# Performance work log

Hardware: AMD Instinct MI355X
Metric: run time of the kernel (lower is better)

The kernel has to match this reference:

```python
import jax, jax.numpy as jnp
import numpy as np

N_HEAD = 16
NEG_INF = -1e30  # finite mask value, safe for softmax/grad


def setup_inputs() -> dict:
    key = jax.random.key(0)
    k1, k2, k3 = jax.random.split(key, 3)
    B, T, C = 4, 2049, 1024
    x = jax.random.normal(k1, (B, T, C), dtype=jnp.float32)
    W_attn = jax.random.normal(k2, (C, 3 * C), dtype=jnp.float32) * (1.0 / np.sqrt(C))
    W_proj = jax.random.normal(k3, (C, C), dtype=jnp.float32) * (1.0 / np.sqrt(C))
    return {"x": x, "W_attn": W_attn, "W_proj": W_proj}


def reference(x, W_attn, W_proj):
    B, T, C = x.shape
    H = N_HEAD
    D = C // H
    qkv = x @ W_attn                                  # (B, T, 3C)
    q, k, v = jnp.split(qkv, 3, axis=-1)
    q = q.reshape(B, T, H, D).transpose(0, 2, 1, 3)   # (B, H, T, D)
    k = k.reshape(B, T, H, D).transpose(0, 2, 1, 3)
    v = v.reshape(B, T, H, D).transpose(0, 2, 1, 3)
    # hybrid mask: causal tril, but state token (row 0) attends to ALL positions
    mask = jnp.tril(jnp.ones((T, T), dtype=bool))
    mask = mask.at[0, :].set(True)
    scale = 1.0 / np.sqrt(D)
    scores = jnp.einsum('bhtd,bhsd->bhts', q, k) * scale
    scores = jnp.where(mask[None, None, :, :], scores, NEG_INF)
    att = jax.nn.softmax(scores, axis=-1)
    y = jnp.einsum('bhts,bhsd->bhtd', att, v)         # (B, H, T, D)
    y = y.transpose(0, 2, 1, 3).reshape(B, T, C)
    return y @ W_proj
```

## Files before the change

kernel.cpp:

```cpp
#include <hip/hip_runtime.h>

typedef __attribute__((ext_vector_type(8))) __bf16 bf16x8;
typedef __attribute__((ext_vector_type(4))) __bf16 bf16x4;
typedef __attribute__((ext_vector_type(4))) float f32x4;
typedef __attribute__((ext_vector_type(16))) float f32x16;

#define GLDS(g, l) __builtin_amdgcn_global_load_lds( \
    (__attribute__((address_space(1))) void*)(void*)(g), \
    (__attribute__((address_space(3))) void*)(void*)(l), 16, 0, 0)

constexpr int T_REAL = 2049;
constexpr int Tp     = 2112;
constexpr int Mreal  = 8196;
constexpr int Mp     = 8448;
constexpr int GK     = 1024;

constexpr float QSCALE = 0.125f * 1.4426950408889634f;

__global__ __launch_bounds__(256)
void prep(const float* __restrict__ x, __bf16* __restrict__ xb,
          const float* __restrict__ Wa, __bf16* __restrict__ WaT,
          const float* __restrict__ Wp, __bf16* __restrict__ WpT) {
    __shared__ float tile[64][65];
    const int z = blockIdx.x;
    if (z < 8448) {
        size_t i = ((size_t)z * 256 + threadIdx.x) * 4;
        float4 v = make_float4(0.f, 0.f, 0.f, 0.f);
        if (i < (size_t)Mreal * GK) v = *(const float4*)(x + i);
        bf16x4 o;
        o.x = (__bf16)v.x; o.y = (__bf16)v.y; o.z = (__bf16)v.z; o.w = (__bf16)v.w;
        *(bf16x4*)(xb + i) = o;
        return;
    }
    const float* W; __bf16* Wt; int N, idx;
    if (z < 9216) { W = Wa; Wt = WaT; N = 3072; idx = z - 8448; }
    else          { W = Wp; Wt = WpT; N = 1024; idx = z - 9216; }
    const int ntiles = N >> 6;
    const int n0 = (idx % ntiles) * 64, k0 = (idx / ntiles) * 64;
    const int tx = threadIdx.x & 63, ty = threadIdx.x >> 6;
#pragma unroll
    for (int j = 0; j < 16; j++) {
        int rk = ty + j * 4;
        tile[rk][tx] = W[(size_t)(k0 + rk) * N + n0 + tx];
    }
    __syncthreads();
#pragma unroll
    for (int j = 0; j < 16; j++) {
        int rn = ty + j * 4;
        Wt[(size_t)(n0 + rn) * GK + k0 + tx] = (__bf16)tile[tx][rn];
    }
}

__global__ __launch_bounds__(256) void transpose_v(const __bf16* __restrict__ v,
                                                   __bf16* __restrict__ vT) {
    __shared__ __bf16 tl[64][72];
    const int bh = blockIdx.y, t0 = blockIdx.x * 64;
    const int tid = threadIdx.x;
    const __bf16* src = v + ((size_t)bh * Tp + t0) * 64;
    {
        const int r = tid >> 3, c = (tid & 7) * 8;
        *(bf16x8*)&tl[r][c]      = *(const bf16x8*)(src + r * 64 + c);
        *(bf16x8*)&tl[r + 32][c] = *(const bf16x8*)(src + (r + 32) * 64 + c);
    }
    __syncthreads();
    __bf16* dst = vT + (size_t)bh * 64 * Tp + t0;
    {
        const int d = tid >> 3, tc = (tid & 7) * 8;
        bf16x8 a, b;
#pragma unroll
        for (int i = 0; i < 8; i++) {
            a[i] = tl[tc + i][d];
            b[i] = tl[tc + i][d + 32];
        }
        *(bf16x8*)(dst + (size_t)d * Tp + tc)        = a;
        *(bf16x8*)(dst + (size_t)(d + 32) * Tp + tc) = b;
    }
}

__global__ __launch_bounds__(512)
void gemm256(const __bf16* __restrict__ A, const __bf16* __restrict__ Bt,
             __bf16* __restrict__ qout, __bf16* __restrict__ kout,
             __bf16* __restrict__ vout) {
    __shared__ __align__(16) __bf16 As[2][16384];
    __shared__ __align__(16) __bf16 Bs[2][16384];

    const int tid = threadIdx.x, lane = tid & 63, w = tid >> 6;
    const int wr = w >> 2, wc = w & 3;
    const int quad = lane >> 4, l15 = lane & 15, l7 = l15 & 7;
    const int m0 = blockIdx.y * 256, n0 = blockIdx.x * 256;

    const int sr = tid >> 3;
    const int sc = ((tid & 7) ^ (sr & 7)) * 8;
    const __bf16* ag = A  + (size_t)(m0 + sr) * GK + sc;
    const __bf16* bg = Bt + (size_t)(n0 + sr) * GK + sc;
    const int ldst = tid * 8;

#define STG_A(T, h) do { const __bf16* s_ = ag + (size_t)(h) * 128 * GK + (T) * 64; \
    GLDS(s_, &As[(T) & 1][(h) * 8192 + ldst]); \
    GLDS(s_ + (size_t)64 * GK, &As[(T) & 1][(h) * 8192 + 4096 + ldst]); } while (0)
#define STG_B(T, h) do { const __bf16* s_ = bg + (size_t)(h) * 128 * GK + (T) * 64; \
    GLDS(s_, &Bs[(T) & 1][(h) * 8192 + ldst]); \
    GLDS(s_ + (size_t)64 * GK, &Bs[(T) & 1][(h) * 8192 + 4096 + ldst]); } while (0)

    f32x4 acc[8][4] = {};
    bf16x8 a[8], b0[4], b1[4];

    STG_A(0, 0); STG_B(0, 1); STG_A(0, 1); STG_B(0, 0); STG_A(1, 0); STG_B(1, 1);
    asm volatile("s_waitcnt vmcnt(4)" ::: "memory");
    __builtin_amdgcn_s_barrier();

    constexpr int NT = GK / 64;

#pragma unroll 1
    for (int T = 0; T < NT; ++T) {
        const int p = T & 1;

#pragma unroll
        for (int f = 0; f < 4; ++f) {
            const int R = f * 32 + wr * 16 + l15;
            a[f * 2 + 0] = *(const bf16x8*)&As[p][R * 64 + ((quad ^ l7) * 8)];
            a[f * 2 + 1] = *(const bf16x8*)&As[p][R * 64 + (((4 + quad) ^ l7) * 8)];
        }
#pragma unroll
        for (int n = 0; n < 2; ++n) {
            const int R = n * 64 + wc * 16 + l15;
            b0[n * 2 + 0] = *(const bf16x8*)&Bs[p][R * 64 + ((quad ^ l7) * 8)];
            b0[n * 2 + 1] = *(const bf16x8*)&Bs[p][R * 64 + (((4 + quad) ^ l7) * 8)];
        }
        if (T + 1 < NT) { STG_A(T + 1, 1); STG_B(T + 1, 0); }
        __builtin_amdgcn_s_barrier();
        asm volatile("s_waitcnt lgkmcnt(0)" ::: "memory");
        __builtin_amdgcn_sched_barrier(0);
        __builtin_amdgcn_s_setprio(1);
#pragma unroll
        for (int f = 0; f < 4; ++f)
#pragma unroll
            for (int n = 0; n < 2; ++n) {
                acc[f][n] = __builtin_amdgcn_mfma_f32_16x16x32_bf16(a[f*2+0], b0[n*2+0], acc[f][n], 0, 0, 0);
                acc[f][n] = __builtin_amdgcn_mfma_f32_16x16x32_bf16(a[f*2+1], b0[n*2+1], acc[f][n], 0, 0, 0);
            }
        __builtin_amdgcn_s_setprio(0);
        __builtin_amdgcn_s_barrier();

#pragma unroll
        for (int n = 0; n < 2; ++n) {
            const int R = 128 + n * 64 + wc * 16 + l15;
            b1[n * 2 + 0] = *(const bf16x8*)&Bs[p][R * 64 + ((quad ^ l7) * 8)];
            b1[n * 2 + 1] = *(const bf16x8*)&Bs[p][R * 64 + (((4 + quad) ^ l7) * 8)];
        }
        __builtin_amdgcn_s_barrier();
        asm volatile("s_waitcnt lgkmcnt(0)" ::: "memory");
        __builtin_amdgcn_sched_barrier(0);
        __builtin_amdgcn_s_setprio(1);
#pragma unroll
        for (int f = 0; f < 4; ++f)
#pragma unroll
            for (int n = 0; n < 2; ++n) {
                acc[f][2+n] = __builtin_amdgcn_mfma_f32_16x16x32_bf16(a[f*2+0], b1[n*2+0], acc[f][2+n], 0, 0, 0);
                acc[f][2+n] = __builtin_amdgcn_mfma_f32_16x16x32_bf16(a[f*2+1], b1[n*2+1], acc[f][2+n], 0, 0, 0);
            }
        __builtin_amdgcn_s_setprio(0);
        __builtin_amdgcn_s_barrier();

#pragma unroll
        for (int f = 0; f < 4; ++f) {
            const int R = 128 + f * 32 + wr * 16 + l15;
            a[f * 2 + 0] = *(const bf16x8*)&As[p][R * 64 + ((quad ^ l7) * 8)];
            a[f * 2 + 1] = *(const bf16x8*)&As[p][R * 64 + (((4 + quad) ^ l7) * 8)];
        }
        if (T + 2 < NT) STG_A(T + 2, 0);
        __builtin_amdgcn_s_barrier();
        asm volatile("s_waitcnt lgkmcnt(0)" ::: "memory");
        __builtin_amdgcn_sched_barrier(0);
        __builtin_amdgcn_s_setprio(1);
#pragma unroll
        for (int f = 0; f < 4; ++f)
#pragma unroll
            for (int n = 0; n < 2; ++n) {
                acc[4+f][2+n] = __builtin_amdgcn_mfma_f32_16x16x32_bf16(a[f*2+0], b1[n*2+0], acc[4+f][2+n], 0, 0, 0);
                acc[4+f][2+n] = __builtin_amdgcn_mfma_f32_16x16x32_bf16(a[f*2+1], b1[n*2+1], acc[4+f][2+n], 0, 0, 0);
            }
        __builtin_amdgcn_s_setprio(0);
        __builtin_amdgcn_s_barrier();

        if (T + 2 < NT) STG_B(T + 2, 1);
        __builtin_amdgcn_s_barrier();
        asm volatile("s_waitcnt lgkmcnt(0)" ::: "memory");
        __builtin_amdgcn_sched_barrier(0);
        __builtin_amdgcn_s_setprio(1);
#pragma unroll
        for (int f = 0; f < 4; ++f)
#pragma unroll
            for (int n = 0; n < 2; ++n) {
                acc[4+f][n] = __builtin_amdgcn_mfma_f32_16x16x32_bf16(a[f*2+0], b0[n*2+0], acc[4+f][n], 0, 0, 0);
                acc[4+f][n] = __builtin_amdgcn_mfma_f32_16x16x32_bf16(a[f*2+1], b0[n*2+1], acc[4+f][n], 0, 0, 0);
            }
        __builtin_amdgcn_s_setprio(0);
        if (T < NT - 2) { asm volatile("s_waitcnt vmcnt(4)" ::: "memory"); }
        else            { asm volatile("s_waitcnt vmcnt(0)" ::: "memory"); }
        __builtin_amdgcn_s_barrier();
    }
#undef STG_A
#undef STG_B

    const int which = n0 >> 10;
    __bf16* op = (which == 0) ? qout : (which == 1) ? kout : vout;
    const float scl = (which == 0) ? QSCALE : 1.0f;
    __bf16* ep = &As[0][0];
    const int rr = tid >> 4, cc = tid & 15;
#pragma unroll
    for (int f = 0; f < 8; ++f) {
        __syncthreads();
#pragma unroll
        for (int n = 0; n < 4; ++n) {
            const int col = (n & 1) * 64 + wc * 16 + (n >> 1) * 128 + l15;
#pragma unroll
            for (int r = 0; r < 4; ++r)
                ep[(wr * 16 + quad * 4 + r) * 264 + col] = (__bf16)(acc[f][n][r] * scl);
        }
        __syncthreads();
        const int m = m0 + (f & 3) * 32 + (f >> 2) * 128 + rr;
        if (m < Mreal) {
            const int b = m / T_REAL;
            const int t = m - b * T_REAL;
#pragma unroll
            for (int g = 0; g < 2; ++g) {
                const int c8 = (cc + g * 16) * 8;
                bf16x8 vv = *(const bf16x8*)&ep[rr * 264 + c8];
                const int gc = n0 + c8;
                const int h = (gc >> 6) & 15;
                *(bf16x8*)&op[((size_t)(b * 16 + h) * Tp + t) * 64 + (gc & 63)] = vv;
            }
        }
    }
}

template <int EPI>
__global__ __launch_bounds__(256)
void gemm128(const __bf16* __restrict__ A, const __bf16* __restrict__ Bt,
             float* __restrict__ outp,
             __bf16* __restrict__ qout, __bf16* __restrict__ kout,
             __bf16* __restrict__ vout) {
    __shared__ __bf16 As[128 * 64];
    __shared__ __bf16 Bs[128 * 64];

    const int tid = threadIdx.x, lane = tid & 63, w = tid >> 6;
    const int wr = w >> 1, wc = w & 1;
    const int quad = lane >> 4, l15 = lane & 15, l7 = l15 & 7;
    const int m0 = blockIdx.y * 128, n0 = blockIdx.x * 128;

    const int row0 = w * 32 + (lane >> 3);
    const int gc8 = ((lane & 7) ^ ((lane >> 3) & 7)) * 8;
    const __bf16* agp = A + (size_t)(m0 + row0) * GK + gc8;
    const __bf16* bgp = Bt + (size_t)(n0 + row0) * GK + gc8;
    __bf16* lap = &As[(w * 256 + lane) * 8];
    __bf16* lbp = &Bs[(w * 256 + lane) * 8];

    f32x4 acc[4][4] = {};

    for (int k0 = 0; k0 < GK; k0 += 64) {
#pragma unroll
        for (int s = 0; s < 4; s++) {
            GLDS(agp + (size_t)s * 8 * GK + k0, lap + s * 512);
            GLDS(bgp + (size_t)s * 8 * GK + k0, lbp + s * 512);
        }
        __syncthreads();
#pragma unroll
        for (int kk = 0; kk < 2; kk++) {
            bf16x8 fa[4], fb[4];
#pragma unroll
            for (int i = 0; i < 4; i++)
                fa[i] = *(const bf16x8*)&As[(wr * 64 + i * 16 + l15) * 64 + (((kk * 4 + quad) ^ l7) * 8)];
#pragma unroll
            for (int j = 0; j < 4; j++)
                fb[j] = *(const bf16x8*)&Bs[(wc * 64 + j * 16 + l15) * 64 + (((kk * 4 + quad) ^ l7) * 8)];
#pragma unroll
            for (int i = 0; i < 4; i++)
#pragma unroll
                for (int j = 0; j < 4; j++)
                    acc[i][j] = __builtin_amdgcn_mfma_f32_16x16x32_bf16(fa[i], fb[j], acc[i][j], 0, 0, 0);
        }
        __syncthreads();
    }

    if constexpr (EPI == 0) {
        const int which = n0 >> 10;
        const int h = ((n0 + wc * 64) >> 6) & 15;
        __bf16* op = (which == 0) ? qout : (which == 1) ? kout : vout;
        const float scl = (which == 0) ? QSCALE : 1.0f;
        __bf16* wls = &As[w * 2048];
#pragma unroll
        for (int p = 0; p < 2; p++) {
            if (p) __syncthreads();
#pragma unroll
            for (int i2 = 0; i2 < 2; i2++)
#pragma unroll
                for (int j = 0; j < 4; j++)
#pragma unroll
                    for (int r = 0; r < 4; r++) {
                        const int lrow = i2 * 16 + quad * 4 + r;
                        const int cX = (j * 2 + (l15 >> 3)) ^ (lrow & 7);
                        wls[lrow * 64 + cX * 8 + (l15 & 7)] =
                            (__bf16)(acc[p * 2 + i2][j][r] * scl);
                    }
            __syncthreads();
#pragma unroll
            for (int it = 0; it < 4; it++) {
                const int lrow = (lane >> 3) + it * 8;
                bf16x8 vv = *(const bf16x8*)&wls[lrow * 64 + (((lane & 7) ^ (lrow & 7)) * 8)];
                const int m = m0 + wr * 64 + p * 32 + lrow;
                if (m < Mreal) {
                    const int b = m / T_REAL;
                    const int t = m - b * T_REAL;
                    *(bf16x8*)&op[(((size_t)(b * 16 + h)) * Tp + t) * 64 + (lane & 7) * 8] = vv;
                }
            }
        }
    } else {
        float* wlf = (float*)&As[0] + w * 1024;
#pragma unroll
        for (int p = 0; p < 4; p++) {
            if (p) __syncthreads();
#pragma unroll
            for (int j = 0; j < 4; j++)
#pragma unroll
                for (int r = 0; r < 4; r++) {
                    const int lrow = quad * 4 + r;
                    const int cX = (j * 4 + (l15 >> 2)) ^ (lrow & 7);
                    wlf[lrow * 64 + cX * 4 + (l15 & 3)] = acc[p][j][r];
                }
            __syncthreads();
#pragma unroll
            for (int it = 0; it < 4; it++) {
                const int lrow = lane >> 2;
                const int c = (lane & 3) + it * 4;
                f32x4 vv = *(const f32x4*)&wlf[lrow * 64 + ((c ^ (lrow & 7)) * 4)];
                const int m = m0 + wr * 64 + p * 16 + lrow;
                if (m < Mreal)
                    *(f32x4*)&outp[(size_t)m * 1024 + n0 + wc * 64 + c * 4] = vv;
            }
        }
    }
}

__global__ __launch_bounds__(256, 4)
void attn(const __bf16* __restrict__ q, const __bf16* __restrict__ kk,
          const __bf16* __restrict__ vT, __bf16* __restrict__ y) {
    __shared__ __bf16 Ks[2][64 * 64];
    __shared__ __bf16 Vs[2][64 * 64];

    static const int QA[17] = {0,31,29,27,25,23,21,19,17,15,13,11,9,7,5,3,1};
    static const int QB[17] = {32,30,28,26,24,22,20,18,16,14,12,10,8,6,4,2,-1};

    const int tid = threadIdx.x, lane = tid & 63, w = tid >> 6;
    const int l31 = lane & 31, hi = lane >> 5, l7 = l31 & 7;
    const int z = blockIdx.x;
    const int slot = z >> 6, zz = z & 63;
    const int bh = (zz & 7) * 8 + (zz >> 3);

    const int qtA = QA[slot];
    const int qt = (w < 2) ? qtA : QB[slot];
    const bool active = qt >= 0;
    const int qts = active ? qt : 0;
    const int qg = qts * 64 + (w & 1) * 32 + l31;
    const int myNt = (qts == 0) ? 32 : qts;
    const int ntmaxB = (qtA == 0) ? 32 : qtA;

    const __bf16* kgb = kk + (size_t)bh * Tp * 64;
    const __bf16* vgb = vT + (size_t)bh * 64 * Tp;
    const int b = bh >> 4, h = bh & 15;

    const int sr = lane >> 3;
    const int scol = ((lane & 7) ^ sr) * 8;
    const int rk = w * 16 + sr;
    const int ldk = w * 1024 + lane * 8;

    bf16x8 qa[4];
    {
        const __bf16* qp = q + ((size_t)bh * Tp + qg) * 64 + hi * 8;
#pragma unroll
        for (int s = 0; s < 4; ++s) qa[s] = *(const bf16x8*)(qp + s * 16);
    }

    f32x16 o0 = {}, o1 = {};
    float mrow = -3e38f, lrow = 0.f;

#define STG_KV(NT_, BUF_) do { \
    const size_t ko_ = (size_t)(NT_) * 4096, vo_ = (size_t)(NT_) * 64; \
    GLDS(kgb + ko_ + rk * 64 + scol,               &Ks[BUF_][ldk]); \
    GLDS(kgb + ko_ + (rk + 8) * 64 + scol,         &Ks[BUF_][ldk + 512]); \
    GLDS(vgb + vo_ + (size_t)rk * Tp + scol,       &Vs[BUF_][ldk]); \
    GLDS(vgb + vo_ + (size_t)(rk + 8) * Tp + scol, &Vs[BUF_][ldk + 512]); } while (0)

    STG_KV(0, 0);
    STG_KV(1, 1);

#pragma unroll 1
    for (int nt = 0; nt <= ntmaxB; ++nt) {
        const int cur = nt & 1;
        if (nt < ntmaxB) { asm volatile("s_waitcnt vmcnt(4)" ::: "memory"); }
        else             { asm volatile("s_waitcnt vmcnt(0)" ::: "memory"); }
        __builtin_amdgcn_s_barrier();
        asm volatile("" ::: "memory");

        if (active && nt <= myNt) {
            const int kv0 = nt * 64;

            f32x16 s0 = {}, s1 = {};
#pragma unroll
            for (int sl = 0; sl < 4; ++sl) {
                const int ch = ((sl * 2 + hi) ^ l7) * 8;
                bf16x8 k0 = *(const bf16x8*)&Ks[cur][l31 * 64 + ch];
                bf16x8 k1 = *(const bf16x8*)&Ks[cur][(32 + l31) * 64 + ch];
                s0 = __builtin_amdgcn_mfma_f32_32x32x16_bf16(k0, qa[sl], s0, 0, 0, 0);
                s1 = __builtin_amdgcn_mfma_f32_32x32x16_bf16(k1, qa[sl], s1, 0, 0, 0);
            }

            if (nt >= qts) {
#pragma unroll
                for (int t = 0; t < 16; ++t) {
                    const int kvg = kv0 + (t & 3) + 8 * (t >> 2) + 4 * hi;
                    const bool v0 = (kvg <= qg) || (qg == 0 && kvg < T_REAL);
                    const bool v1 = (kvg + 32 <= qg) || (qg == 0 && kvg + 32 < T_REAL);
                    s0[t] = v0 ? s0[t] : -1e30f;
                    s1[t] = v1 ? s1[t] : -1e30f;
                }
            }

            float mx = -3e38f;
#pragma unroll
            for (int t = 0; t < 16; ++t) {
                mx = fmaxf(mx, s0[t]);
                mx = fmaxf(mx, s1[t]);
            }
            mx = fmaxf(mx, __shfl_xor(mx, 32));
            if (!__all(mx - mrow <= 8.0f)) {
                const float mn = fmaxf(mrow, mx);
                const float alpha = __builtin_amdgcn_exp2f(mrow - mn);
                mrow = mn;
                lrow *= alpha;
#pragma unroll
                for (int t = 0; t < 16; ++t) { o0[t] *= alpha; o1[t] *= alpha; }
            }

            float rs = 0.f;
#pragma unroll
            for (int t = 0; t < 16; ++t) {
                s0[t] = __builtin_amdgcn_exp2f(s0[t] - mrow);
                s1[t] = __builtin_amdgcn_exp2f(s1[t] - mrow);
                rs += s0[t] + s1[t];
            }
            rs += __shfl_xor(rs, 32);
            lrow += rs;

#pragma unroll
            for (int m = 0; m < 4; ++m) {
                const f32x16 sb = (m & 2) ? s1 : s0;
                constexpr int SB8[4] = {0, 8, 0, 8};
                const int s8 = SB8[m];
                unsigned a01, a23, a45, a67;
                asm("v_cvt_pk_bf16_f32 %0, %1, %2" : "=v"(a01) : "v"(sb[s8 + 0]), "v"(sb[s8 + 1]));
                asm("v_cvt_pk_bf16_f32 %0, %1, %2" : "=v"(a23) : "v"(sb[s8 + 2]), "v"(sb[s8 + 3]));
                asm("v_cvt_pk_bf16_f32 %0, %1, %2" : "=v"(a45) : "v"(sb[s8 + 4]), "v"(sb[s8 + 5]));
                asm("v_cvt_pk_bf16_f32 %0, %1, %2" : "=v"(a67) : "v"(sb[s8 + 6]), "v"(sb[s8 + 7]));
                asm("v_permlane32_swap_b32 %0, %1" : "+v"(a01), "+v"(a45));
                asm("v_permlane32_swap_b32 %0, %1" : "+v"(a23), "+v"(a67));
                union { unsigned u[4]; bf16x8 v; } pf;
                pf.u[0] = a01; pf.u[1] = a23; pf.u[2] = a45; pf.u[3] = a67;
                const int ch = ((m * 2 + hi) ^ l7) * 8;
                bf16x8 v0 = *(const bf16x8*)&Vs[cur][l31 * 64 + ch];
                bf16x8 v1 = *(const bf16x8*)&Vs[cur][(32 + l31) * 64 + ch];
                o0 = __builtin_amdgcn_mfma_f32_32x32x16_bf16(v0, pf.v, o0, 0, 0, 0);
                o1 = __builtin_amdgcn_mfma_f32_32x32x16_bf16(v1, pf.v, o1, 0, 0, 0);
            }
        }

        asm volatile("" ::: "memory");
        __builtin_amdgcn_s_barrier();
        asm volatile("" ::: "memory");
        if (nt + 2 <= ntmaxB) STG_KV(nt + 2, cur);
    }
#undef STG_KV

    if (active && qg < T_REAL) {
        const float inv = 1.0f / lrow;
        __bf16* yp = y + ((size_t)(b * T_REAL + qg)) * 1024 + h * 64 + hi * 4;
#pragma unroll
        for (int g = 0; g < 4; ++g) {
            bf16x4 w0, w1;
            w0.x = (__bf16)(o0[g * 4 + 0] * inv);
            w0.y = (__bf16)(o0[g * 4 + 1] * inv);
            w0.z = (__bf16)(o0[g * 4 + 2] * inv);
            w0.w = (__bf16)(o0[g * 4 + 3] * inv);
            w1.x = (__bf16)(o1[g * 4 + 0] * inv);
            w1.y = (__bf16)(o1[g * 4 + 1] * inv);
            w1.z = (__bf16)(o1[g * 4 + 2] * inv);
            w1.w = (__bf16)(o1[g * 4 + 3] * inv);
            *(bf16x4*)(yp + g * 8)      = w0;
            *(bf16x4*)(yp + 32 + g * 8) = w1;
        }
    }
}

extern "C" void kernel_launch(void* const* d_in, const int* in_sizes, int n_in,
                              void* d_out, int out_size, void* d_ws, size_t ws_size,
                              hipStream_t stream) {
    const float* x  = (const float*)d_in[0];
    const float* Wa = (const float*)d_in[1];
    const float* Wp = (const float*)d_in[2];
    float* out = (float*)d_out;

    char* ws = (char*)d_ws;
    constexpr size_t SZ_XB  = (size_t)Mp * GK * 2;
    constexpr size_t SZ_WAT = (size_t)3072 * GK * 2;
    constexpr size_t SZ_WPT = (size_t)1024 * GK * 2;
    constexpr size_t SZ_QK  = (size_t)64 * Tp * 64 * 2;
    __bf16* xb   = (__bf16*)(ws);
    __bf16* WaT  = (__bf16*)(ws + SZ_XB);
    __bf16* WpT  = (__bf16*)(ws + SZ_XB + SZ_WAT);
    __bf16* qb   = (__bf16*)(ws + SZ_XB + SZ_WAT + SZ_WPT);
    __bf16* kb   = (__bf16*)(ws + SZ_XB + SZ_WAT + SZ_WPT + SZ_QK);
    __bf16* vTb  = (__bf16*)(ws + SZ_XB + SZ_WAT + SZ_WPT + 2 * SZ_QK);
    __bf16* shrd = (__bf16*)(ws + SZ_XB + SZ_WAT + SZ_WPT + 3 * SZ_QK);
    __bf16* vpre = shrd;
    __bf16* yb   = shrd;

    prep<<<9472, 256, 0, stream>>>(x, xb, Wa, WaT, Wp, WpT);
    gemm256<<<dim3(12, 33), 512, 0, stream>>>(xb, WaT, qb, kb, vpre);
    transpose_v<<<dim3(33, 64), 256, 0, stream>>>(vpre, vTb);
    attn<<<1088, 256, 0, stream>>>(qb, kb, vTb, yb);
    gemm128<1><<<dim3(8, 65), 256, 0, stream>>>(yb, WpT, out, nullptr, nullptr, nullptr);
}
```

Before: 273.6 us.

## Batch QKV epilogue staging, trim state-row work, tree-reduce softmax, add MFMA priority

The QKV GEMM epilogue now stages four accumulator fragments at a time into both LDS tiles, so it needs fewer barriers. In attention, the odd warp of query tile 0 no longer processes every KV tile, because only row 0 of that tile needs the full sequence. The max and sum reductions in softmax become tree reductions with shorter dependency chains. s_setprio is raised around the MFMA sections. The batched epilogue relies on the combined As/Bs buffers being large enough, and the skipped work relies on the odd warp's rows all following the causal limit.

```diff
diff --git a/kernel.cpp b/kernel.cpp
--- a/kernel.cpp
+++ b/kernel.cpp
@@ -206,30 +206,41 @@
     const int which = n0 >> 10;
     __bf16* op = (which == 0) ? qout : (which == 1) ? kout : vout;
     const float scl = (which == 0) ? QSCALE : 1.0f;
-    __bf16* ep = &As[0][0];
+    __bf16* const eb0 = &As[0][0];
+    __bf16* const eb1 = &Bs[0][0];
     const int rr = tid >> 4, cc = tid & 15;
 #pragma unroll
-    for (int f = 0; f < 8; ++f) {
+    for (int f4 = 0; f4 < 2; ++f4) {
         __syncthreads();
 #pragma unroll
-        for (int n = 0; n < 4; ++n) {
-            const int col = (n & 1) * 64 + wc * 16 + (n >> 1) * 128 + l15;
-#pragma unroll
-            for (int r = 0; r < 4; ++r)
-                ep[(wr * 16 + quad * 4 + r) * 264 + col] = (__bf16)(acc[f][n][r] * scl);
+        for (int j4 = 0; j4 < 4; ++j4) {
+            const int f = f4 * 4 + j4;
+            __bf16* rg = ((j4 & 2) ? eb1 : eb0) + (j4 & 1) * 8448;
+#pragma unroll
+            for (int n = 0; n < 4; ++n) {
+                const int col = (n & 1) * 64 + wc * 16 + (n >> 1) * 128 + l15;
+#pragma unroll
+                for (int r = 0; r < 4; ++r)
+                    rg[(wr * 16 + quad * 4 + r) * 264 + col] = (__bf16)(acc[f][n][r] * scl);
+            }
         }
         __syncthreads();
-        const int m = m0 + (f & 3) * 32 + (f >> 2) * 128 + rr;
-        if (m < Mreal) {
-            const int b = m / T_REAL;
-            const int t = m - b * T_REAL;
-#pragma unroll
-            for (int g = 0; g < 2; ++g) {
-                const int c8 = (cc + g * 16) * 8;
-                bf16x8 vv = *(const bf16x8*)&ep[rr * 264 + c8];
-                const int gc = n0 + c8;
-                const int h = (gc >> 6) & 15;
-                *(bf16x8*)&op[((size_t)(b * 16 + h) * Tp + t) * 64 + (gc & 63)] = vv;
+#pragma unroll
+        for (int j4 = 0; j4 < 4; ++j4) {
+            const int f = f4 * 4 + j4;
+            const __bf16* rg = ((j4 & 2) ? eb1 : eb0) + (j4 & 1) * 8448;
+            const int m = m0 + (f & 3) * 32 + (f >> 2) * 128 + rr;
+            if (m < Mreal) {
+                const int b = m / T_REAL;
+                const int t = m - b * T_REAL;
+#pragma unroll
+                for (int g = 0; g < 2; ++g) {
+                    const int c8 = (cc + g * 16) * 8;
+                    bf16x8 vv = *(const bf16x8*)&rg[rr * 264 + c8];
+                    const int gc = n0 + c8;
+                    const int h = (gc >> 6) & 15;
+                    *(bf16x8*)&op[((size_t)(b * 16 + h) * Tp + t) * 64 + (gc & 63)] = vv;
+                }
             }
         }
     }
@@ -363,7 +374,7 @@
     const bool active = qt >= 0;
     const int qts = active ? qt : 0;
     const int qg = qts * 64 + (w & 1) * 32 + l31;
-    const int myNt = (qts == 0) ? 32 : qts;
+    const int myNt = (qts == 0) ? ((w & 1) ? 0 : 32) : qts;
     const int ntmaxB = (qtA == 0) ? 32 : qtA;
 
     const __bf16* kgb = kk + (size_t)bh * Tp * 64;
@@ -407,6 +418,7 @@
             const int kv0 = nt * 64;
 
             f32x16 s0 = {}, s1 = {};
+            __builtin_amdgcn_s_setprio(1);
 #pragma unroll
             for (int sl = 0; sl < 4; ++sl) {
                 const int ch = ((sl * 2 + hi) ^ l7) * 8;
@@ -415,6 +427,7 @@
                 s0 = __builtin_amdgcn_mfma_f32_32x32x16_bf16(k0, qa[sl], s0, 0, 0, 0);
                 s1 = __builtin_amdgcn_mfma_f32_32x32x16_bf16(k1, qa[sl], s1, 0, 0, 0);
             }
+            __builtin_amdgcn_s_setprio(0);
 
             if (nt >= qts) {
 #pragma unroll
@@ -427,13 +440,15 @@
                 }
             }
 
-            float mx = -3e38f;
-#pragma unroll
-            for (int t = 0; t < 16; ++t) {
-                mx = fmaxf(mx, s0[t]);
-                mx = fmaxf(mx, s1[t]);
-            }
-            mx = fmaxf(mx, __shfl_xor(mx, 32));
+            float tm[8];
+#pragma unroll
+            for (int t = 0; t < 8; ++t)
+                tm[t] = fmaxf(fmaxf(s0[t], s1[t]), fmaxf(s0[t + 8], s1[t + 8]));
+#pragma unroll
+            for (int st = 4; st > 0; st >>= 1)
+#pragma unroll
+                for (int t = 0; t < st; ++t) tm[t] = fmaxf(tm[t], tm[t + st]);
+            float mx = fmaxf(tm[0], __shfl_xor(tm[0], 32));
             if (!__all(mx - mrow <= 8.0f)) {
                 const float mn = fmaxf(mrow, mx);
                 const float alpha = __builtin_amdgcn_exp2f(mrow - mn);
@@ -443,16 +458,22 @@
                 for (int t = 0; t < 16; ++t) { o0[t] *= alpha; o1[t] *= alpha; }
             }
 
-            float rs = 0.f;
-#pragma unroll
-            for (int t = 0; t < 16; ++t) {
-                s0[t] = __builtin_amdgcn_exp2f(s0[t] - mrow);
-                s1[t] = __builtin_amdgcn_exp2f(s1[t] - mrow);
-                rs += s0[t] + s1[t];
-            }
-            rs += __shfl_xor(rs, 32);
-            lrow += rs;
-
+            float tr[8];
+#pragma unroll
+            for (int t = 0; t < 8; ++t) {
+                s0[t]     = __builtin_amdgcn_exp2f(s0[t] - mrow);
+                s1[t]     = __builtin_amdgcn_exp2f(s1[t] - mrow);
+                s0[t + 8] = __builtin_amdgcn_exp2f(s0[t + 8] - mrow);
+                s1[t + 8] = __builtin_amdgcn_exp2f(s1[t + 8] - mrow);
+                tr[t] = (s0[t] + s1[t]) + (s0[t + 8] + s1[t + 8]);
+            }
+#pragma unroll
+            for (int st = 4; st > 0; st >>= 1)
+#pragma unroll
+                for (int t = 0; t < st; ++t) tr[t] += tr[t + st];
+            lrow += tr[0] + __shfl_xor(tr[0], 32);
+
+            __builtin_amdgcn_s_setprio(1);
 #pragma unroll
             for (int m = 0; m < 4; ++m) {
                 const f32x16 sb = (m & 2) ? s1 : s0;
@@ -473,6 +494,7 @@
                 o0 = __builtin_amdgcn_mfma_f32_32x32x16_bf16(v0, pf.v, o0, 0, 0, 0);
                 o1 = __builtin_amdgcn_mfma_f32_32x32x16_bf16(v1, pf.v, o1, 0, 0, 0);
             }
+            __builtin_amdgcn_s_setprio(0);
         }
 
         asm volatile("" ::: "memory");
```

Measured after the change: 278.6 us. Within noise of the previous version (+1.8%).
